# Kernel tuning notes

Measured on AMD Instinct MI355X. Metric: run time of the kernel, lower is better.

The kernel has to match this reference:

```python
import jax, jax.numpy as jnp
import numpy as np

B, N, R, D, K, T = 256, 2048, 64, 64, 2, 8  # graphs, nodes, roots, embed dim, in-degree, node types


def setup_inputs() -> dict:
    key = jax.random.key(0)
    k_root, k_w1, k_w2, k_types = jax.random.split(key, 4)
    rng = np.random.default_rng(0)
    # topologically valid DAG: parents of node i are drawn from [0, i)
    raw = rng.integers(0, 1 << 30, size=(B, N, K))
    denom = np.maximum(np.arange(N), 1)[None, :, None]
    node_inputs_indices = (raw % denom).astype(np.int32)
    node_types = jax.random.randint(k_types, (B, N), 0, T, dtype=jnp.int32)
    root_embeddings = jax.random.normal(k_root, (B, R, D), dtype=jnp.float32)
    # per-node-type encoder MLP: [K*D -> 2D -> D], GELU between layers
    W1 = jax.random.normal(k_w1, (T, K * D, 2 * D), dtype=jnp.float32) / np.sqrt(K * D)
    b1 = jnp.zeros((T, 2 * D), dtype=jnp.float32)
    W2 = jax.random.normal(k_w2, (T, 2 * D, D), dtype=jnp.float32) / np.sqrt(2 * D)
    b2 = jnp.zeros((T, D), dtype=jnp.float32)
    return {
        "root_embeddings": root_embeddings,
        "W1": W1,
        "b1": b1,
        "W2": W2,
        "b2": b2,
        "node_inputs_indices": jnp.asarray(node_inputs_indices),
        "node_types": node_types,
    }


def reference(root_embeddings, W1, b1, W2, b2, node_inputs_indices, node_types):
    buf0 = jnp.zeros((B, N, D), dtype=root_embeddings.dtype)
    buf0 = buf0.at[:, :R].set(root_embeddings)
    # per-step data for the sequential traversal over nodes R..N-1
    idx_seq = jnp.transpose(node_inputs_indices[:, R:, :], (1, 0, 2))  # [N-R, B, K]
    typ_seq = jnp.transpose(node_types[:, R:], (1, 0))                  # [N-R, B]
    pos_seq = jnp.arange(R, N)

    def step(buf, xs):
        idx, typ, pos = xs
        # gather parent embeddings: [B, K, D]
        parents = jnp.take_along_axis(buf, idx[:, :, None], axis=1)
        x = parents.reshape(B, K * D)
        h = jax.nn.gelu(jnp.einsum("bi,bih->bh", x, W1[typ]) + b1[typ], approximate=False)
        out = jnp.einsum("bh,bhd->bd", h, W2[typ]) + b2[typ]  # [B, D]
        buf = buf.at[:, pos].set(out)
        return buf, None

    buf, _ = jax.lax.scan(step, buf0, (idx_seq, typ_seq, pos_seq))
    return buf  # [B, N, D] full embeddings buffer
```

## Files before the change

kernel.cpp:

```cpp
#include <hip/hip_runtime.h>
#include <hip/hip_bf16.h>
#include <math.h>

#define NB 256
#define NN 2048
#define NR 64
#define ND 64
#define NT 8
#define NTH 512
#define NW 8
#define XP 136

typedef __attribute__((ext_vector_type(8))) short short8;
typedef __attribute__((ext_vector_type(4))) float f32x4;

__device__ __forceinline__ unsigned short f2bf(float f) {
    unsigned u = __float_as_uint(f);
    return (unsigned short)((u + 0x7fffu + ((u >> 16) & 1u)) >> 16);
}

__device__ __forceinline__ unsigned pk2bf(float a, float b) {
    __hip_bfloat162 h = __float22bfloat162_rn(float2{a, b});
    unsigned r; __builtin_memcpy(&r, &h, 4); return r;
}

__device__ __forceinline__ float fast_gelu(float v) {
    const float x  = v * 0.70710678118654752f;
    const float ax = fabsf(x);
    const float t  = __builtin_amdgcn_rcpf(fmaf(0.3275911f, ax, 1.0f));
    float p = fmaf(1.061405429f, t, -1.453152027f);
    p = fmaf(p, t, 1.421413741f);
    p = fmaf(p, t, -0.284496736f);
    p = fmaf(p, t, 0.254829592f);
    p *= t;
    const float e       = exp2f(ax * ax * -1.4426950408889634f);
    const float erf_abs = fmaf(-p, e, 1.0f);
    const float er      = copysignf(erf_abs, v);
    return 0.5f * v * (1.0f + er);
}

__global__ void convert_weights(const float* __restrict__ W1,
                                const float* __restrict__ W2,
                                unsigned short* __restrict__ w1t,
                                unsigned short* __restrict__ w2t) {
    int g = blockIdx.x * 256 + threadIdx.x;
    if (g < NT * 128 * 128) {
        int t = g >> 14, r = g & 16383, j = r >> 7, i = r & 127;
        w1t[g] = f2bf(W1[(t * 128 + i) * 128 + j]);
    }
    if (g < NT * 64 * 128) {
        int t = g >> 13, r = g & 8191, d = r >> 7, jj = r & 127;
        w2t[g] = f2bf(W2[(t * 128 + jj) * 64 + d]);
    }
}

__device__ __forceinline__ void block_scan2048(unsigned* __restrict__ arr,
                                               unsigned* __restrict__ csum,
                                               int w, int lane) {
    for (int c = w; c < 32; c += NW) {
        unsigned v = arr[c * 64 + lane];
        #pragma unroll
        for (int off = 1; off < 64; off <<= 1) {
            unsigned u = __shfl_up(v, off, 64);
            if (lane >= off) v += u;
        }
        arr[c * 64 + lane] = v;
        if (lane == 63) csum[c] = v;
    }
    __syncthreads();
    if (w == 0) {
        unsigned s = (lane < 32) ? csum[lane] : 0u;
        #pragma unroll
        for (int off = 1; off < 32; off <<= 1) {
            unsigned u = __shfl_up(s, off, 64);
            if (lane >= off) s += u;
        }
        if (lane < 32) csum[lane] = s;
    }
    __syncthreads();
    for (int c = w; c < 32; c += NW)
        if (c > 0) arr[c * 64 + lane] += csum[c - 1];
    __syncthreads();
}

__global__ __launch_bounds__(NTH, 2)
void dag_encoder_kernel(const float* __restrict__ roots,
                        const float* __restrict__ b1,
                        const float* __restrict__ b2,
                        const int*   __restrict__ idxs,
                        const int*   __restrict__ types,
                        float* __restrict__ out,
                        const unsigned short* __restrict__ w1t,
                        const unsigned short* __restrict__ w2t)
{
    __shared__ unsigned int   depth[NN];
    __shared__ unsigned short keys[NN];
    __shared__ unsigned int   scanA[NN];
    __shared__ unsigned short list[NN];
    __shared__ unsigned int   listP[NN];
    __shared__ __align__(4) unsigned short parv[2 * NN];
    __shared__ unsigned int   csum[32];
    __shared__ __align__(16) unsigned short hs[NW][16][XP];
    __shared__ int s_maxd;

    const int b    = blockIdx.x;
    const int tid  = threadIdx.x;
    const int w    = tid >> 6;
    const int lane = tid & 63;
    const int q    = lane >> 4;
    const int l    = lane & 15;

    float* gbuf = out + (size_t)b * NN * ND;
    const int* gtyp = types + (size_t)b * NN;
    const int* gi   = idxs  + (size_t)b * NN * 2;

    {
        const float4* r4 = (const float4*)(roots + (size_t)b * NR * ND);
        float4* o4 = (float4*)gbuf;
        for (int i = tid; i < NR * ND / 4; i += NTH) o4[i] = r4[i];
        for (int i = tid; i < 2 * NN; i += NTH) parv[i] = (unsigned short)gi[i];
        for (int i = tid; i < NN; i += NTH) depth[i] = (i < NR) ? 0u : 0xFFFFFFFFu;
        for (int i = tid; i < NN; i += NTH) scanA[i] = 0;
        if (tid == 0) s_maxd = 0;
    }
    __syncthreads();

    if (w == 0) {
        for (int g0 = NR; g0 < NN; g0 += 64) {
            const int n  = g0 + lane;
            const int p0 = parv[2 * n];
            const int p1 = parv[2 * n + 1];
            bool done = false;
            #pragma unroll 1
            for (int iter = 0; iter < 64; ++iter) {
                if (!done) {
                    const unsigned d0 = depth[p0];
                    const unsigned d1 = depth[p1];
                    if (d0 != 0xFFFFFFFFu && d1 != 0xFFFFFFFFu) {
                        depth[n] = 1u + (d0 > d1 ? d0 : d1);
                        done = true;
                    }
                }
                if (__all(done)) break;
                asm volatile("s_waitcnt lgkmcnt(0)" ::: "memory");
            }
        }
    }
    __syncthreads();

    {
        unsigned mloc = 0;
        for (int i = tid; i < NN; i += NTH) {
            if (i >= NR) {
                unsigned lv = depth[i]; if (lv > 255u) lv = 255u;
                if (lv > mloc) mloc = lv;
                int key = (int)lv * 8 + gtyp[i];
                keys[i] = (unsigned short)key;
                atomicAdd(&scanA[key], 1u);
            }
        }
        atomicMax(&s_maxd, (int)mloc);
    }
    __syncthreads();

    block_scan2048(scanA, csum, w, lane);

    for (int i = tid; i < NN; i += NTH) depth[i] = (i == 0) ? 0u : scanA[i - 1];
    __syncthreads();

    for (int i = tid; i < NN; i += NTH) {
        if (i >= NR) {
            unsigned p = atomicAdd(&depth[keys[i]], 1u);
            list[p]  = (unsigned short)i;
            listP[p] = ((const unsigned*)parv)[i];
        }
    }
    __syncthreads();

    short8 w1f[32];
    #pragma unroll
    for (int n0 = 0; n0 < 8; ++n0)
        #pragma unroll
        for (int kk = 0; kk < 4; ++kk)
            w1f[n0 * 4 + kk] = *(const short8*)(w1t +
                ((size_t)(w * 128 + n0 * 16 + l) * 128 + kk * 32 + q * 8));
    short8 w2f[16];
    #pragma unroll
    for (int n0 = 0; n0 < 4; ++n0)
        #pragma unroll
        for (int kk = 0; kk < 4; ++kk)
            w2f[n0 * 4 + kk] = *(const short8*)(w2t +
                ((size_t)(w * 64 + n0 * 16 + l) * 128 + kk * 32 + q * 8));
    float bv1[8], bv2[4];
    #pragma unroll
    for (int n = 0; n < 8; ++n) bv1[n] = b1[w * 128 + n * 16 + l];
    #pragma unroll
    for (int n = 0; n < 4; ++n) bv2[n] = b2[w * 64 + n * 16 + l];

    const int maxd = s_maxd;
    for (int L = 1; L <= maxd; ++L) {
        const int key = L * 8 + w;
        const unsigned seg = scanA[key - 1];
        const int cnt = (int)(scanA[key] - seg);
        for (int r0 = 0; r0 < cnt; r0 += 16) {
            const int rows = min(16, cnt - r0);

            const int rr = min(l, rows - 1);
            const unsigned pcat = listP[seg + r0 + rr];
            const int p0 = (int)(pcat & 0xFFFFu), p1 = (int)(pcat >> 16);

            float4 ga[8];
            #pragma unroll
            for (int kk = 0; kk < 4; ++kk) {
                const float* s = gbuf + (size_t)(kk < 2 ? p0 : p1) * 64 + (kk & 1) * 32 + q * 8;
                ga[2 * kk]     = *(const float4*)s;
                ga[2 * kk + 1] = *(const float4*)(s + 4);
            }
            short8 af[4];
            #pragma unroll
            for (int kk = 0; kk < 4; ++kk) {
                union { short8 s; unsigned u[4]; } v;
                v.u[0] = pk2bf(ga[2 * kk].x,     ga[2 * kk].y);
                v.u[1] = pk2bf(ga[2 * kk].z,     ga[2 * kk].w);
                v.u[2] = pk2bf(ga[2 * kk + 1].x, ga[2 * kk + 1].y);
                v.u[3] = pk2bf(ga[2 * kk + 1].z, ga[2 * kk + 1].w);
                af[kk] = v.s;
            }

            #pragma unroll
            for (int h = 0; h < 2; ++h) {
                f32x4 c1[4];
                #pragma unroll
                for (int n0 = 0; n0 < 4; ++n0) c1[n0] = (f32x4){0.f, 0.f, 0.f, 0.f};
                #pragma unroll
                for (int kk = 0; kk < 4; ++kk)
                    #pragma unroll
                    for (int n0 = 0; n0 < 4; ++n0)
                        c1[n0] = __builtin_amdgcn_mfma_f32_16x16x32_bf16(
                            af[kk], w1f[(h * 4 + n0) * 4 + kk], c1[n0], 0, 0, 0);

                #pragma unroll
                for (int n0 = 0; n0 < 4; ++n0) {
                    const float bv = bv1[h * 4 + n0];
                    #pragma unroll
                    for (int rg = 0; rg < 4; ++rg) {
                        const float v = c1[n0][rg] + bv;
                        hs[w][q * 4 + rg][(h * 4 + n0) * 16 + l] = f2bf(fast_gelu(v));
                    }
                }
            }
            asm volatile("s_waitcnt lgkmcnt(0)" ::: "memory");

            short8 a2[4];
            #pragma unroll
            for (int kk = 0; kk < 4; ++kk)
                a2[kk] = *(const short8*)&hs[w][l][kk * 32 + q * 8];
            f32x4 c2[4];
            #pragma unroll
            for (int n0 = 0; n0 < 4; ++n0) c2[n0] = (f32x4){0.f, 0.f, 0.f, 0.f};
            #pragma unroll
            for (int kk = 0; kk < 4; ++kk)
                #pragma unroll
                for (int n0 = 0; n0 < 4; ++n0)
                    c2[n0] = __builtin_amdgcn_mfma_f32_16x16x32_bf16(
                        a2[kk], w2f[n0 * 4 + kk], c2[n0], 0, 0, 0);

            #pragma unroll
            for (int n0 = 0; n0 < 4; ++n0) {
                const float bv = bv2[n0];
                #pragma unroll
                for (int rg = 0; rg < 4; ++rg) {
                    const int row = q * 4 + rg;
                    if (row < rows) {
                        const int nd = list[seg + r0 + row];
                        gbuf[nd * 64 + n0 * 16 + l] = c2[n0][rg] + bv;
                    }
                }
            }
        }
        __syncthreads();
    }
}

extern "C" void kernel_launch(void* const* d_in, const int* in_sizes, int n_in,
                              void* d_out, int out_size, void* d_ws, size_t ws_size,
                              hipStream_t stream) {
    const float* roots = (const float*)d_in[0];
    const float* W1    = (const float*)d_in[1];
    const float* b1    = (const float*)d_in[2];
    const float* W2    = (const float*)d_in[3];
    const float* b2    = (const float*)d_in[4];
    const int*   idxs  = (const int*)d_in[5];
    const int*   types = (const int*)d_in[6];
    float*       outp  = (float*)d_out;

    unsigned short* w1t = (unsigned short*)d_ws;
    unsigned short* w2t = w1t + NT * 128 * 128;

    convert_weights<<<dim3(512), dim3(256), 0, stream>>>(W1, W2, w1t, w2t);
    dag_encoder_kernel<<<dim3(NB), dim3(NTH), 0, stream>>>(
        roots, b1, b2, idxs, types, outp, w1t, w2t);
}
```

Measured before the change: 336.0 us.

## Stash previous-level outputs in LDS, prefetch next-level parents, cheaper GELU

Each level's outputs are now also written as bf16 into a double-buffered shared-memory stash indexed by position within the level. Next-level parent gathers read from the stash when the parent sits at the immediately preceding depth, instead of making a latency-bound global round-trip. Parents of the next level's first tile that are already complete are prefetched from global memory into registers at the end of each level. GELU switches to a shorter erf polynomial. The extra shared memory (a new cursor array plus the stash) likely removes the second resident block per CU, and the GELU approximation is less accurate.

New measurement: 481.3 us. 1.43x slower.

```diff
diff --git a/kernel.cpp b/kernel.cpp
--- a/kernel.cpp
+++ b/kernel.cpp
@@ -10,6 +10,8 @@
 #define NTH 512
 #define NW 8
 #define XP 136
+#define SROWS 256
+#define SP 72
 
 typedef __attribute__((ext_vector_type(8))) short short8;
 typedef __attribute__((ext_vector_type(4))) float f32x4;
@@ -24,19 +26,24 @@
     unsigned r; __builtin_memcpy(&r, &h, 4); return r;
 }
 
+__device__ __forceinline__ short8 cvt8(float4 a, float4 b) {
+    union { short8 s; unsigned u[4]; } v;
+    v.u[0] = pk2bf(a.x, a.y); v.u[1] = pk2bf(a.z, a.w);
+    v.u[2] = pk2bf(b.x, b.y); v.u[3] = pk2bf(b.z, b.w);
+    return v.s;
+}
+
 __device__ __forceinline__ float fast_gelu(float v) {
-    const float x  = v * 0.70710678118654752f;
-    const float ax = fabsf(x);
-    const float t  = __builtin_amdgcn_rcpf(fmaf(0.3275911f, ax, 1.0f));
-    float p = fmaf(1.061405429f, t, -1.453152027f);
-    p = fmaf(p, t, 1.421413741f);
-    p = fmaf(p, t, -0.284496736f);
-    p = fmaf(p, t, 0.254829592f);
+    const float ax = fabsf(v) * 0.70710678118654752f;
+    const float t  = __builtin_amdgcn_rcpf(fmaf(0.47047f, ax, 1.0f));
+    float p = fmaf(0.7478556f, t, -0.0958798f);
+    p = fmaf(p, t, 0.3480242f);
     p *= t;
-    const float e       = exp2f(ax * ax * -1.4426950408889634f);
-    const float erf_abs = fmaf(-p, e, 1.0f);
-    const float er      = copysignf(erf_abs, v);
-    return 0.5f * v * (1.0f + er);
+    const float e  = exp2f(ax * ax * -1.4426950408889634f);
+    const float er = fmaf(-p, e, 1.0f);
+    const float es = copysignf(er, v);
+    const float hv = 0.5f * v;
+    return fmaf(hv, es, hv);
 }
 
 __global__ void convert_weights(const float* __restrict__ W1,
@@ -96,11 +103,13 @@
     __shared__ unsigned int   depth[NN];
     __shared__ unsigned short keys[NN];
     __shared__ unsigned int   scanA[NN];
+    __shared__ unsigned int   curs[NN];
     __shared__ unsigned short list[NN];
     __shared__ unsigned int   listP[NN];
     __shared__ __align__(4) unsigned short parv[2 * NN];
     __shared__ unsigned int   csum[32];
     __shared__ __align__(16) unsigned short hs[NW][16][XP];
+    __shared__ __align__(16) unsigned short stash[2][SROWS][SP];
     __shared__ int s_maxd;
 
     const int b    = blockIdx.x;
@@ -165,14 +174,15 @@
 
     block_scan2048(scanA, csum, w, lane);
 
-    for (int i = tid; i < NN; i += NTH) depth[i] = (i == 0) ? 0u : scanA[i - 1];
+    for (int i = tid; i < NN; i += NTH) curs[i] = (i == 0) ? 0u : scanA[i - 1];
     __syncthreads();
 
     for (int i = tid; i < NN; i += NTH) {
         if (i >= NR) {
-            unsigned p = atomicAdd(&depth[keys[i]], 1u);
+            unsigned p = atomicAdd(&curs[keys[i]], 1u);
             list[p]  = (unsigned short)i;
             listP[p] = ((const unsigned*)parv)[i];
+            keys[i]  = (unsigned short)p;
         }
     }
     __syncthreads();
@@ -197,34 +207,63 @@
     #pragma unroll
     for (int n = 0; n < 4; ++n) bv2[n] = b2[w * 64 + n * 16 + l];
 
+    float4 pf[8];
+    bool pff0 = false, pff1 = false;
+
     const int maxd = s_maxd;
     for (int L = 1; L <= maxd; ++L) {
         const int key = L * 8 + w;
         const unsigned seg = scanA[key - 1];
         const int cnt = (int)(scanA[key] - seg);
+        const unsigned lvlbaseCur  = scanA[L * 8 - 1];
+        const unsigned lvlbasePrev = (L >= 2) ? scanA[L * 8 - 9] : 0u;
+
         for (int r0 = 0; r0 < cnt; r0 += 16) {
             const int rows = min(16, cnt - r0);
+            const bool usePF = (r0 == 0) && (L >= 2);
 
             const int rr = min(l, rows - 1);
             const unsigned pcat = listP[seg + r0 + rr];
             const int p0 = (int)(pcat & 0xFFFFu), p1 = (int)(pcat >> 16);
 
-            float4 ga[8];
-            #pragma unroll
-            for (int kk = 0; kk < 4; ++kk) {
-                const float* s = gbuf + (size_t)(kk < 2 ? p0 : p1) * 64 + (kk & 1) * 32 + q * 8;
-                ga[2 * kk]     = *(const float4*)s;
-                ga[2 * kk + 1] = *(const float4*)(s + 4);
-            }
             short8 af[4];
-            #pragma unroll
-            for (int kk = 0; kk < 4; ++kk) {
-                union { short8 s; unsigned u[4]; } v;
-                v.u[0] = pk2bf(ga[2 * kk].x,     ga[2 * kk].y);
-                v.u[1] = pk2bf(ga[2 * kk].z,     ga[2 * kk].w);
-                v.u[2] = pk2bf(ga[2 * kk + 1].x, ga[2 * kk + 1].y);
-                v.u[3] = pk2bf(ga[2 * kk + 1].z, ga[2 * kk + 1].w);
-                af[kk] = v.s;
+            {
+                bool hot = false; int slot = 0;
+                if (p0 >= NR && depth[p0] == (unsigned)(L - 1)) {
+                    slot = (int)keys[p0] - (int)lvlbasePrev;
+                    hot = (slot < SROWS);
+                }
+                if (hot) {
+                    const unsigned short* sp = &stash[(L - 1) & 1][slot][0];
+                    af[0] = *(const short8*)(sp + q * 8);
+                    af[1] = *(const short8*)(sp + 32 + q * 8);
+                } else if (usePF && pff0) {
+                    af[0] = cvt8(pf[0], pf[1]);
+                    af[1] = cvt8(pf[2], pf[3]);
+                } else {
+                    const float* s = gbuf + (size_t)p0 * 64 + q * 8;
+                    af[0] = cvt8(*(const float4*)s,        *(const float4*)(s + 4));
+                    af[1] = cvt8(*(const float4*)(s + 32), *(const float4*)(s + 36));
+                }
+            }
+            {
+                bool hot = false; int slot = 0;
+                if (p1 >= NR && depth[p1] == (unsigned)(L - 1)) {
+                    slot = (int)keys[p1] - (int)lvlbasePrev;
+                    hot = (slot < SROWS);
+                }
+                if (hot) {
+                    const unsigned short* sp = &stash[(L - 1) & 1][slot][0];
+                    af[2] = *(const short8*)(sp + q * 8);
+                    af[3] = *(const short8*)(sp + 32 + q * 8);
+                } else if (usePF && pff1) {
+                    af[2] = cvt8(pf[4], pf[5]);
+                    af[3] = cvt8(pf[6], pf[7]);
+                } else {
+                    const float* s = gbuf + (size_t)p1 * 64 + q * 8;
+                    af[2] = cvt8(*(const float4*)s,        *(const float4*)(s + 4));
+                    af[3] = cvt8(*(const float4*)(s + 32), *(const float4*)(s + 36));
+                }
             }
 
             #pragma unroll
@@ -265,6 +304,7 @@
                     c2[n0] = __builtin_amdgcn_mfma_f32_16x16x32_bf16(
                         a2[kk], w2f[n0 * 4 + kk], c2[n0], 0, 0, 0);
 
+            const int slotB = (int)(seg - lvlbaseCur) + r0;
             #pragma unroll
             for (int n0 = 0; n0 < 4; ++n0) {
                 const float bv = bv2[n0];
@@ -273,8 +313,38 @@
                     const int row = q * 4 + rg;
                     if (row < rows) {
                         const int nd = list[seg + r0 + row];
-                        gbuf[nd * 64 + n0 * 16 + l] = c2[n0][rg] + bv;
+                        const float val = c2[n0][rg] + bv;
+                        gbuf[nd * 64 + n0 * 16 + l] = val;
+                        const int sw = slotB + row;
+                        if (sw < SROWS)
+                            stash[L & 1][sw][n0 * 16 + l] = f2bf(val);
                     }
+                }
+            }
+        }
+
+        pff0 = pff1 = false;
+        if (L + 1 <= maxd) {
+            const int keyN = key + 8;
+            const unsigned segN = scanA[keyN - 1];
+            const int cntN = (int)(scanA[keyN] - segN);
+            if (cntN > 0) {
+                const int rrN = min(l, min(cntN, 16) - 1);
+                const unsigned pcatN = listP[segN + rrN];
+                const int pn0 = (int)(pcatN & 0xFFFFu), pn1 = (int)(pcatN >> 16);
+                const unsigned dn0 = (pn0 >= NR) ? depth[pn0] : 0u;
+                const unsigned dn1 = (pn1 >= NR) ? depth[pn1] : 0u;
+                if (dn0 <= (unsigned)(L - 1)) {
+                    const float* s = gbuf + (size_t)pn0 * 64 + q * 8;
+                    pf[0] = *(const float4*)s;        pf[1] = *(const float4*)(s + 4);
+                    pf[2] = *(const float4*)(s + 32); pf[3] = *(const float4*)(s + 36);
+                    pff0 = true;
+                }
+                if (dn1 <= (unsigned)(L - 1)) {
+                    const float* s = gbuf + (size_t)pn1 * 64 + q * 8;
+                    pf[4] = *(const float4*)s;        pf[5] = *(const float4*)(s + 4);
+                    pf[6] = *(const float4*)(s + 32); pf[7] = *(const float4*)(s + 36);
+                    pff1 = true;
                 }
             }
         }
```
